# Kernel optimization log

Measured on AMD Instinct MI355X. Metric: run time of the kernel, lower is better.

The kernel has to match this reference:

```python
import jax, jax.numpy as jnp
import numpy as np

B, L, D, H, N_LAYERS = 32, 512, 1024, 1024, 4

def setup_inputs() -> dict:
    key = jax.random.key(0)
    ks = jax.random.split(key, 3)
    x = jax.random.normal(ks[0], (B, L, D), dtype=jnp.float32)
    h0 = jnp.zeros((N_LAYERS, B, H), dtype=jnp.float32)
    # Xavier-normal init: std = sqrt(2/(fan_in+fan_out))
    std = float(np.sqrt(2.0 / (H + H)))
    WI = jax.random.normal(ks[1], (N_LAYERS, H, H), dtype=jnp.float32) * std  # layer 0 uses D==H
    WH = jax.random.normal(ks[2], (N_LAYERS, H, H), dtype=jnp.float32) * std
    BI = jnp.zeros((N_LAYERS, H), dtype=jnp.float32)
    BH = jnp.zeros((N_LAYERS, H), dtype=jnp.float32)
    return {"x": x, "h0": h0, "WI": WI, "BI": BI, "WH": WH, "BH": BH}

def reference(x, h0, WI, BI, WH, BH):
    n_layers = WI.shape[0]

    def step(h_prev, x_t):
        # h_prev: [n_layers, B, H]; x_t: [B, D]
        inp = x_t
        hs = []
        for l in range(n_layers):
            h_new = jnp.tanh(inp @ WI[l].T + BI[l] + h_prev[l] @ WH[l].T + BH[l])
            hs.append(h_new)
            inp = h_new
        h = jnp.stack(hs, axis=0)
        return h, hs[-1]

    xs = jnp.swapaxes(x, 0, 1)  # [L, B, D]
    h_final, out = jax.lax.scan(step, h0, xs)
    output = jnp.swapaxes(out, 0, 1)  # [B, L, H]
    return output, h_final
```

## Files before the change

kernel.cpp:

```cpp
#include <hip/hip_runtime.h>
#include <hip/hip_fp16.h>

#define BB 32
#define LL 512
#define HH 1024
#define NL 4
#define TPL 16
#define CPB 64
#define TAGM 0x0001000100010001ULL
#define SROW 1032

typedef unsigned long long ull;
typedef _Float16 f16x8 __attribute__((ext_vector_type(8)));
typedef float    f32x4 __attribute__((ext_vector_type(4)));

__device__ __forceinline__ f16x8 cvt8(const float* __restrict__ p) {
  f32x4 lo = *reinterpret_cast<const f32x4*>(p);
  f32x4 hi = *reinterpret_cast<const f32x4*>(p + 4);
  f16x8 r;
#pragma unroll
  for (int e = 0; e < 4; ++e) { r[e] = (_Float16)lo[e]; r[e + 4] = (_Float16)hi[e]; }
  return r;
}

__device__ __forceinline__ ull tag_bad(f16x8 v, ull want) {
  union { f16x8 v; ull u[2]; } c; c.v = v;
  return ((c.u[0] ^ want) | (c.u[1] ^ want)) & TAGM;
}

__device__ __forceinline__ f16x8 fix_q(const _Float16* __restrict__ gsrc, ull want) {
  const ull* p = reinterpret_cast<const ull*>(gsrc);
  union { ull u[2]; f16x8 v; } c;
  do {
    c.u[0] = __hip_atomic_load(p, __ATOMIC_RELAXED, __HIP_MEMORY_SCOPE_AGENT);
  } while ((c.u[0] ^ want) & TAGM);
  do {
    c.u[1] = __hip_atomic_load(p + 1, __ATOMIC_RELAXED, __HIP_MEMORY_SCOPE_AGENT);
  } while ((c.u[1] ^ want) & TAGM);
  return c.v;
}

__global__ __launch_bounds__(512, 1) void rnn_persist(
    const float* __restrict__ x,
    const float* __restrict__ h0,
    const float* __restrict__ WI,
    const float* __restrict__ BI,
    const float* __restrict__ WH,
    const float* __restrict__ BH,
    float* __restrict__ out,
    _Float16* __restrict__ hbuf,
    unsigned* __restrict__ pflag,
    int rsmask, int rshift) {
  const int l = blockIdx.x & 7;
  if (l >= NL) return;
  const int tile = blockIdx.x >> 3;
  const int c0   = tile * CPB;
  const int tid  = threadIdx.x;
  const int w    = tid >> 6;
  const int lane = tid & 63;
  const int crow = lane & 15;
  const int kgrp = lane >> 4;

  extern __shared__ char smem[];
  _Float16* sIn  = (_Float16*)smem;
  _Float16* sHid = sIn + 32 * SROW;
  float*    redp = (float*)smem;
#define RED(W2, R, C) redp[(((W2) * 32 + (R)) * 68) + (C)]

  f16x8 wIf[4][4], wHf[4][4];
  {
    const float* WIb = WI + (size_t)l * HH * HH;
    const float* WHb = WH + (size_t)l * HH * HH;
#pragma unroll
    for (int ct = 0; ct < 4; ++ct) {
      const size_t row = (size_t)(c0 + ct * 16 + crow) * HH;
#pragma unroll
      for (int j = 0; j < 4; ++j) {
        const int k = w * 128 + kgrp * 8 + j * 32;
        wIf[ct][j] = cvt8(WIb + row + k);
        wHf[ct][j] = cvt8(WHb + row + k);
      }
    }
  }

  const int rb = tid >> 4;
  const int c4 = (tid & 15) * 4;
  float bias4[4];
#pragma unroll
  for (int j = 0; j < 4; ++j)
    bias4[j] = BI[l * HH + c0 + c4 + j] + BH[l * HH + c0 + c4 + j];

  for (int t = 0; t < LL; ++t) {
    const ull wantI = (((t >> rshift) & 1) ^ 1) ? TAGM : 0ULL;
    const ull wantH = ((((t - 1) >> rshift) & 1) ^ 1) ? TAGM : 0ULL;

    if (tid < 48) {
      if (tid < 16) {
        if (l > 0)
          while (__hip_atomic_load(&pflag[(l - 1) * TPL + tid], __ATOMIC_RELAXED,
                                   __HIP_MEMORY_SCOPE_AGENT) < (unsigned)(t + 1))
            __builtin_amdgcn_s_sleep(1);
      } else if (tid >= 32) {
        const int Lt = tid - 32;
        if (l < NL - 1 && t > rsmask)
          while (__hip_atomic_load(&pflag[(l + 1) * TPL + Lt], __ATOMIC_RELAXED,
                                   __HIP_MEMORY_SCOPE_AGENT) < (unsigned)(t - rsmask))
            __builtin_amdgcn_s_sleep(1);
      }
    }
    __syncthreads();

    if (tid == 0 && t > 0)
      __hip_atomic_store(&pflag[l * TPL + tile], (unsigned)t, __ATOMIC_RELAXED,
                         __HIP_MEMORY_SCOPE_AGENT);

    const _Float16* srcI =
        hbuf + ((size_t)(l - 1) * (rsmask + 1) + (t & rsmask)) * BB * HH;
    const _Float16* srcH =
        hbuf + ((size_t)l * (rsmask + 1) + ((t - 1) & rsmask)) * BB * HH;

    {
      f16x8 tq[8];
      if (l == 0) {
#pragma unroll
        for (int it = 0; it < 8; ++it) {
          const int q = it * 512 + tid, row = q >> 7, col = (q & 127) * 8;
          tq[it] = cvt8(x + ((size_t)row * LL + t) * HH + col);
        }
      } else {
#pragma unroll
        for (int it = 0; it < 8; ++it) {
          const int q = it * 512 + tid, row = q >> 7, col = (q & 127) * 8;
          tq[it] = *reinterpret_cast<const f16x8*>(srcI + (size_t)row * HH + col);
        }
        ull badI = 0;
#pragma unroll
        for (int it = 0; it < 8; ++it) badI |= tag_bad(tq[it], wantI);
        if (badI) {
#pragma unroll
          for (int it = 0; it < 8; ++it) {
            const int q = it * 512 + tid, row = q >> 7, col = (q & 127) * 8;
            if (tag_bad(tq[it], wantI))
              tq[it] = fix_q(srcI + (size_t)row * HH + col, wantI);
          }
        }
      }
#pragma unroll
      for (int it = 0; it < 8; ++it) {
        const int q = it * 512 + tid, row = q >> 7, col = (q & 127) * 8;
        *reinterpret_cast<f16x8*>(&sIn[(size_t)row * SROW + col]) = tq[it];
      }
    }

    {
      f16x8 tq[8];
      if (t == 0) {
#pragma unroll
        for (int it = 0; it < 8; ++it) {
          const int q = it * 512 + tid, row = q >> 7, col = (q & 127) * 8;
          tq[it] = cvt8(h0 + ((size_t)l * BB + row) * HH + col);
        }
      } else {
#pragma unroll
        for (int it = 0; it < 8; ++it) {
          const int q = it * 512 + tid, row = q >> 7, col = (q & 127) * 8;
          tq[it] = *reinterpret_cast<const f16x8*>(srcH + (size_t)row * HH + col);
        }
        ull badH = 0;
#pragma unroll
        for (int it = 0; it < 8; ++it) badH |= tag_bad(tq[it], wantH);
        if (badH) {
#pragma unroll
          for (int it = 0; it < 8; ++it) {
            const int q = it * 512 + tid, row = q >> 7, col = (q & 127) * 8;
            const _Float16* a = srcH + (size_t)row * HH + col;
            int tries = 0;
            while (tag_bad(tq[it], wantH)) {
              if (tries++ < 64) {
                const volatile ull* vp = reinterpret_cast<const volatile ull*>(a);
                ull lo = vp[0], hi = vp[1];
                union { ull u[2]; f16x8 v; } c; c.u[0] = lo; c.u[1] = hi;
                tq[it] = c.v;
              } else {
                tq[it] = fix_q(a, wantH);
              }
            }
          }
        }
      }
#pragma unroll
      for (int it = 0; it < 8; ++it) {
        const int q = it * 512 + tid, row = q >> 7, col = (q & 127) * 8;
        *reinterpret_cast<f16x8*>(&sHid[(size_t)row * SROW + col]) = tq[it];
      }
    }
    __syncthreads();

    f32x4 acc[4][2];
#pragma unroll
    for (int ct = 0; ct < 4; ++ct)
#pragma unroll
      for (int rt = 0; rt < 2; ++rt) acc[ct][rt] = (f32x4){0.f, 0.f, 0.f, 0.f};
#pragma unroll
    for (int j = 0; j < 4; ++j) {
      const int base = w * 128 + kgrp * 8 + j * 32;
      f16x8 ai0 = *reinterpret_cast<const f16x8*>(&sIn [(size_t)crow * SROW + base]);
      f16x8 ai1 = *reinterpret_cast<const f16x8*>(&sIn [(size_t)(16 + crow) * SROW + base]);
      f16x8 ah0 = *reinterpret_cast<const f16x8*>(&sHid[(size_t)crow * SROW + base]);
      f16x8 ah1 = *reinterpret_cast<const f16x8*>(&sHid[(size_t)(16 + crow) * SROW + base]);
#pragma unroll
      for (int ct = 0; ct < 4; ++ct) {
        acc[ct][0] = __builtin_amdgcn_mfma_f32_16x16x32_f16(ai0, wIf[ct][j], acc[ct][0], 0, 0, 0);
        acc[ct][1] = __builtin_amdgcn_mfma_f32_16x16x32_f16(ai1, wIf[ct][j], acc[ct][1], 0, 0, 0);
        acc[ct][0] = __builtin_amdgcn_mfma_f32_16x16x32_f16(ah0, wHf[ct][j], acc[ct][0], 0, 0, 0);
        acc[ct][1] = __builtin_amdgcn_mfma_f32_16x16x32_f16(ah1, wHf[ct][j], acc[ct][1], 0, 0, 0);
      }
    }
    __syncthreads();

#pragma unroll
    for (int ct = 0; ct < 4; ++ct)
#pragma unroll
      for (int rt = 0; rt < 2; ++rt)
#pragma unroll
        for (int r = 0; r < 4; ++r)
          RED(w, rt * 16 + kgrp * 4 + r, ct * 16 + crow) = acc[ct][rt][r];
    __syncthreads();

    float v[4];
#pragma unroll
    for (int j = 0; j < 4; ++j) {
      float s = bias4[j];
#pragma unroll
      for (int w2 = 0; w2 < 8; ++w2) s += RED(w2, rb, c4 + j);
      v[j] = tanhf(s);
    }
    {
      union { _Float16 h[4]; ull u; } pk;
#pragma unroll
      for (int j = 0; j < 4; ++j) pk.h[j] = (_Float16)v[j];
      const ull tg = (((t >> rshift) & 1) ^ 1) ? TAGM : 0ULL;
      pk.u = (pk.u & ~TAGM) | tg;
      const size_t off =
          ((size_t)l * (rsmask + 1) + (t & rsmask)) * BB * HH + (size_t)rb * HH + c0 + c4;
      *reinterpret_cast<ull*>(hbuf + off) = pk.u;
      __hip_atomic_store(reinterpret_cast<ull*>(hbuf + off), pk.u,
                         __ATOMIC_RELAXED, __HIP_MEMORY_SCOPE_AGENT);
    }
    if (l == NL - 1) {
      f32x4 o = {v[0], v[1], v[2], v[3]};
      __builtin_nontemporal_store(
          o, reinterpret_cast<f32x4*>(out + ((size_t)rb * LL + t) * HH + c0 + c4));
    }
    if (t == LL - 1) {
      f32x4 o = {v[0], v[1], v[2], v[3]};
      __builtin_nontemporal_store(
          o, reinterpret_cast<f32x4*>(out + (size_t)BB * LL * HH +
                                      ((size_t)l * BB + rb) * HH + c0 + c4));
    }
  }

  __syncthreads();
  if (tid == 0)
    __hip_atomic_store(&pflag[l * TPL + tile], (unsigned)LL, __ATOMIC_RELAXED,
                       __HIP_MEMORY_SCOPE_AGENT);
#undef RED
}

extern "C" void kernel_launch(void* const* d_in, const int* in_sizes, int n_in,
                              void* d_out, int out_size, void* d_ws, size_t ws_size,
                              hipStream_t stream) {
  const float* x  = (const float*)d_in[0];
  const float* h0 = (const float*)d_in[1];
  const float* WI = (const float*)d_in[2];
  const float* BI = (const float*)d_in[3];
  const float* WH = (const float*)d_in[4];
  const float* BH = (const float*)d_in[5];
  float* out = (float*)d_out;

  const size_t perSlot = (size_t)NL * BB * HH * sizeof(_Float16);
  int rs = 512;
  while (rs > 8 && (size_t)rs * perSlot + 65536 > ws_size) rs >>= 1;
  int rshift = 0;
  while ((1 << rshift) < rs) ++rshift;

  _Float16* hbuf = (_Float16*)d_ws;
  unsigned* pflag = (unsigned*)((char*)d_ws + (size_t)rs * perSlot);

  const int smemBytes = 2 * 32 * SROW * (int)sizeof(_Float16);
  static int attrSet = 0;
  if (!attrSet) {
    hipFuncSetAttribute(reinterpret_cast<const void*>(rnn_persist),
                        hipFuncAttributeMaxDynamicSharedMemorySize, smemBytes);
    attrSet = 1;
  }

  hipMemsetAsync(pflag, 0, (size_t)NL * TPL * sizeof(unsigned), stream);
  rnn_persist<<<128, 512, smemBytes, stream>>>(x, h0, WI, BI, WH, BH, out, hbuf,
                                               pflag, rs - 1, rshift);
}
```

Baseline: 3.502 ms.

## Split hidden-state exchange into plain and atomic buffers, batch loads before tag checks

Each step's hidden output is now written twice: a plain store to one buffer, read for the recurrent input, and a device-scope atomic store to a second buffer, read for the inter-layer input and the fallback path. The input and hidden loads are both issued before any tag validation, so their latencies overlap instead of running one after the other. The aim is to cut the latency of the cross-block hidden-state exchange on the serial critical path. In exchange, workspace use doubles, which may shrink the ring-buffer depth, and every step adds an extra store.

```diff
diff --git a/kernel.cpp b/kernel.cpp
--- a/kernel.cpp
+++ b/kernel.cpp
@@ -48,7 +48,8 @@
     const float* __restrict__ WH,
     const float* __restrict__ BH,
     float* __restrict__ out,
-    _Float16* __restrict__ hbuf,
+    _Float16* __restrict__ hL,
+    _Float16* __restrict__ hM,
     unsigned* __restrict__ pflag,
     int rsmask, int rshift) {
   const int l = blockIdx.x & 7;
@@ -114,85 +115,82 @@
       __hip_atomic_store(&pflag[l * TPL + tile], (unsigned)t, __ATOMIC_RELAXED,
                          __HIP_MEMORY_SCOPE_AGENT);
 
-    const _Float16* srcI =
-        hbuf + ((size_t)(l - 1) * (rsmask + 1) + (t & rsmask)) * BB * HH;
-    const _Float16* srcH =
-        hbuf + ((size_t)l * (rsmask + 1) + ((t - 1) & rsmask)) * BB * HH;
-
-    {
-      f16x8 tq[8];
-      if (l == 0) {
+    const size_t slotI = ((size_t)(l - 1) * (rsmask + 1) + (t & rsmask)) * BB * HH;
+    const size_t slotH = ((size_t)l * (rsmask + 1) + ((t - 1) & rsmask)) * BB * HH;
+    const _Float16* srcIM = hM + slotI;
+    const _Float16* srcHL = hL + slotH;
+    const _Float16* srcHM = hM + slotH;
+
+    f16x8 tqI[8], tqH[8];
+    if (l == 0) {
+#pragma unroll
+      for (int it = 0; it < 8; ++it) {
+        const int q = it * 512 + tid, row = q >> 7, col = (q & 127) * 8;
+        tqI[it] = cvt8(x + ((size_t)row * LL + t) * HH + col);
+      }
+    } else {
+#pragma unroll
+      for (int it = 0; it < 8; ++it) {
+        const int q = it * 512 + tid, row = q >> 7, col = (q & 127) * 8;
+        tqI[it] = *reinterpret_cast<const f16x8*>(srcIM + (size_t)row * HH + col);
+      }
+    }
+    if (t == 0) {
+#pragma unroll
+      for (int it = 0; it < 8; ++it) {
+        const int q = it * 512 + tid, row = q >> 7, col = (q & 127) * 8;
+        tqH[it] = cvt8(h0 + ((size_t)l * BB + row) * HH + col);
+      }
+    } else {
+#pragma unroll
+      for (int it = 0; it < 8; ++it) {
+        const int q = it * 512 + tid, row = q >> 7, col = (q & 127) * 8;
+        tqH[it] = *reinterpret_cast<const f16x8*>(srcHL + (size_t)row * HH + col);
+      }
+    }
+
+    if (t != 0) {
+      ull badH = 0;
+#pragma unroll
+      for (int it = 0; it < 8; ++it) badH |= tag_bad(tqH[it], wantH);
+      if (badH) {
 #pragma unroll
         for (int it = 0; it < 8; ++it) {
           const int q = it * 512 + tid, row = q >> 7, col = (q & 127) * 8;
-          tq[it] = cvt8(x + ((size_t)row * LL + t) * HH + col);
-        }
-      } else {
-#pragma unroll
-        for (int it = 0; it < 8; ++it) {
-          const int q = it * 512 + tid, row = q >> 7, col = (q & 127) * 8;
-          tq[it] = *reinterpret_cast<const f16x8*>(srcI + (size_t)row * HH + col);
-        }
-        ull badI = 0;
-#pragma unroll
-        for (int it = 0; it < 8; ++it) badI |= tag_bad(tq[it], wantI);
-        if (badI) {
-#pragma unroll
-          for (int it = 0; it < 8; ++it) {
-            const int q = it * 512 + tid, row = q >> 7, col = (q & 127) * 8;
-            if (tag_bad(tq[it], wantI))
-              tq[it] = fix_q(srcI + (size_t)row * HH + col, wantI);
-          }
-        }
-      }
-#pragma unroll
-      for (int it = 0; it < 8; ++it) {
-        const int q = it * 512 + tid, row = q >> 7, col = (q & 127) * 8;
-        *reinterpret_cast<f16x8*>(&sIn[(size_t)row * SROW + col]) = tq[it];
-      }
-    }
-
-    {
-      f16x8 tq[8];
-      if (t == 0) {
-#pragma unroll
-        for (int it = 0; it < 8; ++it) {
-          const int q = it * 512 + tid, row = q >> 7, col = (q & 127) * 8;
-          tq[it] = cvt8(h0 + ((size_t)l * BB + row) * HH + col);
-        }
-      } else {
-#pragma unroll
-        for (int it = 0; it < 8; ++it) {
-          const int q = it * 512 + tid, row = q >> 7, col = (q & 127) * 8;
-          tq[it] = *reinterpret_cast<const f16x8*>(srcH + (size_t)row * HH + col);
-        }
-        ull badH = 0;
-#pragma unroll
-        for (int it = 0; it < 8; ++it) badH |= tag_bad(tq[it], wantH);
-        if (badH) {
-#pragma unroll
-          for (int it = 0; it < 8; ++it) {
-            const int q = it * 512 + tid, row = q >> 7, col = (q & 127) * 8;
-            const _Float16* a = srcH + (size_t)row * HH + col;
-            int tries = 0;
-            while (tag_bad(tq[it], wantH)) {
-              if (tries++ < 64) {
-                const volatile ull* vp = reinterpret_cast<const volatile ull*>(a);
-                ull lo = vp[0], hi = vp[1];
-                union { ull u[2]; f16x8 v; } c; c.u[0] = lo; c.u[1] = hi;
-                tq[it] = c.v;
-              } else {
-                tq[it] = fix_q(a, wantH);
-              }
+          const _Float16* aL = srcHL + (size_t)row * HH + col;
+          int tries = 0;
+          while (tag_bad(tqH[it], wantH)) {
+            if (tries++ < 64) {
+              const volatile ull* vp = reinterpret_cast<const volatile ull*>(aL);
+              ull lo = vp[0], hi = vp[1];
+              union { ull u[2]; f16x8 v; } c; c.u[0] = lo; c.u[1] = hi;
+              tqH[it] = c.v;
+            } else {
+              tqH[it] = fix_q(srcHM + (size_t)row * HH + col, wantH);
             }
           }
         }
       }
-#pragma unroll
-      for (int it = 0; it < 8; ++it) {
-        const int q = it * 512 + tid, row = q >> 7, col = (q & 127) * 8;
-        *reinterpret_cast<f16x8*>(&sHid[(size_t)row * SROW + col]) = tq[it];
-      }
+    }
+    if (l != 0) {
+      ull badI = 0;
+#pragma unroll
+      for (int it = 0; it < 8; ++it) badI |= tag_bad(tqI[it], wantI);
+      if (badI) {
+#pragma unroll
+        for (int it = 0; it < 8; ++it) {
+          const int q = it * 512 + tid, row = q >> 7, col = (q & 127) * 8;
+          if (tag_bad(tqI[it], wantI))
+            tqI[it] = fix_q(srcIM + (size_t)row * HH + col, wantI);
+        }
+      }
+    }
+
+#pragma unroll
+    for (int it = 0; it < 8; ++it) {
+      const int q = it * 512 + tid, row = q >> 7, col = (q & 127) * 8;
+      *reinterpret_cast<f16x8*>(&sIn [(size_t)row * SROW + col]) = tqI[it];
+      *reinterpret_cast<f16x8*>(&sHid[(size_t)row * SROW + col]) = tqH[it];
     }
     __syncthreads();
 
@@ -243,8 +241,8 @@
       pk.u = (pk.u & ~TAGM) | tg;
       const size_t off =
           ((size_t)l * (rsmask + 1) + (t & rsmask)) * BB * HH + (size_t)rb * HH + c0 + c4;
-      *reinterpret_cast<ull*>(hbuf + off) = pk.u;
-      __hip_atomic_store(reinterpret_cast<ull*>(hbuf + off), pk.u,
+      *reinterpret_cast<ull*>(hL + off) = pk.u;
+      __hip_atomic_store(reinterpret_cast<ull*>(hM + off), pk.u,
                          __ATOMIC_RELAXED, __HIP_MEMORY_SCOPE_AGENT);
     }
     if (l == NL - 1) {
@@ -280,12 +278,13 @@
 
   const size_t perSlot = (size_t)NL * BB * HH * sizeof(_Float16);
   int rs = 512;
-  while (rs > 8 && (size_t)rs * perSlot + 65536 > ws_size) rs >>= 1;
+  while (rs > 8 && 2 * (size_t)rs * perSlot + 65536 > ws_size) rs >>= 1;
   int rshift = 0;
   while ((1 << rshift) < rs) ++rshift;
 
-  _Float16* hbuf = (_Float16*)d_ws;
-  unsigned* pflag = (unsigned*)((char*)d_ws + (size_t)rs * perSlot);
+  _Float16* hL = (_Float16*)d_ws;
+  _Float16* hM = hL + (size_t)rs * NL * BB * HH;
+  unsigned* pflag = (unsigned*)((char*)d_ws + 2 * (size_t)rs * perSlot);
 
   const int smemBytes = 2 * 32 * SROW * (int)sizeof(_Float16);
   static int attrSet = 0;
@@ -296,6 +295,6 @@
   }
 
   hipMemsetAsync(pflag, 0, (size_t)NL * TPL * sizeof(unsigned), stream);
-  rnn_persist<<<128, 512, smemBytes, stream>>>(x, h0, WI, BI, WH, BH, out, hbuf,
+  rnn_persist<<<128, 512, smemBytes, stream>>>(x, h0, WI, BI, WH, BH, out, hL, hM,
                                                pflag, rs - 1, rshift);
 }
```

After: 4.893 ms. 39.7% more time.
